# Kernel tuning notes

Hardware: AMD Instinct MI355X
Metric: run time of the kernel (lower is better)

## Reference

```python
import jax, jax.numpy as jnp
import numpy as np

B = 1024           # number of drug pairs (graphs per side)
ATOMS = 64         # atoms per molecule
N = B * ATOMS      # total atoms per side
H = 512            # hidden_size * number_of_molecules
FFN_H = 2048
OUT = 86           # num_tasks


def setup_inputs() -> dict:
    key = jax.random.key(0)
    ks = jax.random.split(key, 12)
    inv = 1.0 / np.sqrt(H)
    inv2 = 1.0 / np.sqrt(2 * H)
    invf = 1.0 / np.sqrt(FFN_H)
    return {
        "left_output": jax.random.normal(ks[0], (B, H), jnp.float32),
        "right_output": jax.random.normal(ks[1], (B, H), jnp.float32),
        "left_atom": jax.random.normal(ks[2], (N, H), jnp.float32),
        "right_atom": jax.random.normal(ks[3], (N, H), jnp.float32),
        "left_batch": jnp.arange(N, dtype=jnp.int32) // ATOMS,
        "right_batch": jnp.arange(N, dtype=jnp.int32) // ATOMS,
        "noise": jax.random.uniform(ks[4], (B, H), jnp.float32),
        "w_i_w": jax.random.normal(ks[5], (H, H), jnp.float32) * inv,
        "w_i_b": jnp.zeros((H,), jnp.float32),
        "prj_i_w": jax.random.normal(ks[6], (H, H), jnp.float32) * inv,
        "prj_i_b": jnp.zeros((H,), jnp.float32),
        "ffn1_w": jax.random.normal(ks[7], (2 * H, FFN_H), jnp.float32) * inv2,
        "ffn1_b": jnp.zeros((FFN_H,), jnp.float32),
        "ffn2_w": jax.random.normal(ks[8], (FFN_H, OUT), jnp.float32) * invf,
        "ffn2_b": jnp.zeros((OUT,), jnp.float32),
    }


def _seg_softmax(s, seg, num_segments):
    m = jax.ops.segment_max(s, seg, num_segments=num_segments)
    e = jnp.exp(s - m[seg])
    z = jax.ops.segment_sum(e, seg, num_segments=num_segments)
    return e / z[seg]


def reference(left_output, right_output, left_atom, right_atom,
              left_batch, right_batch, noise,
              w_i_w, w_i_b, prj_i_w, prj_i_b,
              ffn1_w, ffn1_b, ffn2_w, ffn2_b):
    # repeat_interleave(left_output, degree(right_batch)) == gather by segment id
    left_align = left_output[right_batch]    # [N_r, H]
    right_align = right_output[left_batch]   # [N_l, H]

    # cross-molecule coattention scores (elementwise product + reduce)
    left_scores = jnp.sum((left_atom @ w_i_w + w_i_b) * (right_align @ prj_i_w + prj_i_b), axis=-1)
    left_scores = _seg_softmax(left_scores, left_batch, B)
    right_scores = jnp.sum((right_atom @ w_i_w + w_i_b) * (left_align @ prj_i_w + prj_i_b), axis=-1)
    right_scores = _seg_softmax(right_scores, right_batch, B)

    # attention-weighted global add pool
    h_output = jax.ops.segment_sum(left_atom * right_align * left_scores[:, None], left_batch, num_segments=B)
    t_output = jax.ops.segment_sum(right_atom * left_align * right_scores[:, None], right_batch, num_segments=B)

    # sign-directed noise perturbation (same noise for both sides, as in original)
    nrm = jnp.maximum(jnp.linalg.norm(noise, axis=-1, keepdims=True), 1e-12)
    noise_n = noise / nrm
    h_pert = h_output + jnp.sign(h_output) * noise_n * 0.1
    t_pert = t_output + jnp.sign(t_output) * noise_n * 0.1

    pair = jnp.concatenate([h_pert, t_pert], axis=-1)  # [B, 2H]
    hid = jax.nn.relu(pair @ ffn1_w + ffn1_b)
    output = hid @ ffn2_w + ffn2_b  # training mode: raw logits, no sigmoid
    return (output, h_output, h_pert, left_scores, right_scores, left_output, right_output)
```

## Files before the change

kernel.cpp:

```cpp
#include <hip/hip_runtime.h>
#include <hip/hip_bf16.h>

#define B_ 1024
#define H_ 512
#define N_ (B_ * 64)
#define FFN_ 2048
#define OUT_ 86

typedef __bf16 bf16_t;
typedef __attribute__((ext_vector_type(8))) __bf16 bf16x8;
typedef __attribute__((ext_vector_type(4))) float f32x4;

__device__ __forceinline__ float wred_sum(float v) {
#pragma unroll
  for (int m = 32; m; m >>= 1) v += __shfl_xor(v, m);
  return v;
}
__device__ __forceinline__ float wred_max(float v) {
#pragma unroll
  for (int m = 32; m; m >>= 1) v = fmaxf(v, __shfl_xor(v, m));
  return v;
}

__device__ __forceinline__ void gload_lds16(const void* g, void* l) {
  __builtin_amdgcn_global_load_lds((const __attribute__((address_space(1))) unsigned int*)g,
                                   (__attribute__((address_space(3))) unsigned int*)l, 16, 0, 0);
}

__global__ void k_prep(const float* __restrict__ w_i_w, const float* __restrict__ w_i_b,
                       const float* __restrict__ prj_w, const float* __restrict__ prj_b,
                       float* __restrict__ dv, float* __restrict__ ev, float* __restrict__ c0) {
  int b = blockIdx.x, l = threadIdx.x;
  float s = 0.f;
  if (b < 512) {
    for (int h = l; h < H_; h += 64) s += w_i_w[b * H_ + h] * prj_b[h];
    s = wred_sum(s);
    if (l == 0) dv[b] = s;
  } else if (b < 1024) {
    int j = b - 512;
    for (int h = l; h < H_; h += 64) s += prj_w[j * H_ + h] * w_i_b[h];
    s = wred_sum(s);
    if (l == 0) ev[j] = s;
  } else {
    for (int h = l; h < H_; h += 64) s += w_i_b[h] * prj_b[h];
    s = wred_sum(s);
    if (l == 0) c0[0] = s;
  }
}

__global__ void k_cvec(const float* __restrict__ ro, const float* __restrict__ lo,
                       const float* __restrict__ ev, const float* __restrict__ c0,
                       float* __restrict__ cL, float* __restrict__ cR) {
  int b = blockIdx.x, side = blockIdx.y, l = threadIdx.x;
  const float* x = side ? lo : ro;
  float s = 0.f;
  for (int j = l; j < H_; j += 64) s += x[b * H_ + j] * ev[j];
  s = wred_sum(s);
  if (l == 0) (side ? cR : cL)[b] = s + c0[0];
}

template <bool BT, bool BIAS, bool RELU>
__global__ __launch_bounds__(256) void gemm64(const float* __restrict__ A, const float* __restrict__ Bm,
                                              const float* __restrict__ bias, float* __restrict__ C,
                                              int M, int N, int K) {
  __shared__ float As[16][68];
  __shared__ float Bs[16][68];
  const int bm = blockIdx.x * 64, bn = blockIdx.y * 64;
  const int t = threadIdx.x;
  const int tx = t & 15, ty = t >> 4;
  float acc[4][4] = {};
  for (int k0 = 0; k0 < K; k0 += 16) {
#pragma unroll
    for (int i = 0; i < 4; i++) {
      int m = (t >> 4) + i * 16;
      As[t & 15][m] = A[(size_t)(bm + m) * K + k0 + (t & 15)];
    }
    if (BT) {
#pragma unroll
      for (int i = 0; i < 4; i++) {
        int n = (t >> 4) + i * 16;
        Bs[t & 15][n] = Bm[(size_t)(bn + n) * K + k0 + (t & 15)];
      }
    } else {
#pragma unroll
      for (int i = 0; i < 4; i++) {
        int kk = (t >> 6) + i * 4;
        Bs[kk][t & 63] = Bm[(size_t)(k0 + kk) * N + bn + (t & 63)];
      }
    }
    __syncthreads();
#pragma unroll
    for (int kk = 0; kk < 16; kk++) {
      float4 av = *(const float4*)&As[kk][ty * 4];
      float4 bv = *(const float4*)&Bs[kk][tx * 4];
      float a_[4] = {av.x, av.y, av.z, av.w};
      float b_[4] = {bv.x, bv.y, bv.z, bv.w};
#pragma unroll
      for (int i = 0; i < 4; i++)
#pragma unroll
        for (int j = 0; j < 4; j++) acc[i][j] += a_[i] * b_[j];
    }
    __syncthreads();
  }
#pragma unroll
  for (int i = 0; i < 4; i++) {
    int m = bm + ty * 4 + i;
    float tmp[4];
#pragma unroll
    for (int j = 0; j < 4; j++) {
      float x = acc[i][j];
      if (BIAS) x += bias[bn + tx * 4 + j];
      if (RELU) x = fmaxf(x, 0.f);
      tmp[j] = x;
    }
    float4 v;
    v.x = tmp[0]; v.y = tmp[1]; v.z = tmp[2]; v.w = tmp[3];
    *(float4*)&C[(size_t)m * N + bn + tx * 4] = v;
  }
}

__global__ __launch_bounds__(512, 2) void k_atoms(const float* __restrict__ atomL, const float* __restrict__ atomR,
                                                  const float* __restrict__ uL, const float* __restrict__ uR,
                                                  const float* __restrict__ cL, const float* __restrict__ cR,
                                                  float* __restrict__ scoresL, float* __restrict__ scoresR,
                                                  float* __restrict__ pL, float* __restrict__ pR) {
  const int b = blockIdx.x, side = blockIdx.y;
  const float* __restrict__ atom = side ? atomR : atomL;
  const float* __restrict__ u = side ? uR : uL;
  const float cb = (side ? cR : cL)[b];
  float* __restrict__ scores = side ? scoresR : scoresL;
  float* __restrict__ p = side ? pR : pL;

  const int t = threadIdx.x, wave = t >> 6, lane = t & 63;
  const int colA = lane * 4, colB = 256 + lane * 4;

  __shared__ float s_lds[64];
  __shared__ float pp_lds[8][512];

  float a[8][8];
  float ur[8];
  const float* base = atom + ((size_t)b * 64 + wave * 8) * H_;
#pragma unroll
  for (int ai = 0; ai < 8; ai++) {
    *(float4*)&a[ai][0] = *(const float4*)&base[(size_t)ai * H_ + colA];
    *(float4*)&a[ai][4] = *(const float4*)&base[(size_t)ai * H_ + colB];
  }
  *(float4*)&ur[0] = *(const float4*)&u[(size_t)b * H_ + colA];
  *(float4*)&ur[4] = *(const float4*)&u[(size_t)b * H_ + colB];

#pragma unroll
  for (int ai = 0; ai < 8; ai++) {
    float dot = 0.f;
#pragma unroll
    for (int j = 0; j < 8; j++) dot += a[ai][j] * ur[j];
    dot = wred_sum(dot);
    if (lane == 0) s_lds[wave * 8 + ai] = dot + cb;
  }
  __syncthreads();
  if (wave == 0) {
    float s = s_lds[lane];
    float mx = wred_max(s);
    float e = expf(s - mx);
    float z = wred_sum(e);
    float w = e / z;
    s_lds[lane] = w;
    scores[(size_t)b * 64 + lane] = w;
  }
  __syncthreads();
  float pp[8] = {};
#pragma unroll
  for (int ai = 0; ai < 8; ai++) {
    float w = s_lds[wave * 8 + ai];
#pragma unroll
    for (int j = 0; j < 8; j++) pp[j] += w * a[ai][j];
  }
#pragma unroll
  for (int j = 0; j < 4; j++) {
    pp_lds[wave][colA + j] = pp[j];
    pp_lds[wave][colB + j] = pp[4 + j];
  }
  __syncthreads();
  float s = 0.f;
#pragma unroll
  for (int w2 = 0; w2 < 8; w2++) s += pp_lds[w2][t];
  p[(size_t)b * H_ + t] = s;
}

__global__ __launch_bounds__(512) void k_pert(const float* __restrict__ lo, const float* __restrict__ ro,
                                              const float* __restrict__ noise,
                                              const float* __restrict__ pL, const float* __restrict__ pR,
                                              float* __restrict__ h_out, float* __restrict__ h_pert,
                                              bf16_t* __restrict__ pairbf) {
  const int b = blockIdx.x, t = threadIdx.x;
  float nv = noise[(size_t)b * H_ + t];
  float sq = nv * nv;
  sq = wred_sum(sq);
  __shared__ float red[8];
  if ((t & 63) == 0) red[t >> 6] = sq;
  __syncthreads();
  float tot = 0.f;
#pragma unroll
  for (int i = 0; i < 8; i++) tot += red[i];
  float nrm = fmaxf(sqrtf(tot), 1e-12f);
  float nn = nv / nrm * 0.1f;
  float h = ro[(size_t)b * H_ + t] * pL[(size_t)b * H_ + t];
  float tt = lo[(size_t)b * H_ + t] * pR[(size_t)b * H_ + t];
  float sh = (h > 0.f) ? 1.f : ((h < 0.f) ? -1.f : 0.f);
  float st = (tt > 0.f) ? 1.f : ((tt < 0.f) ? -1.f : 0.f);
  float hp = h + sh * nn;
  float tp = tt + st * nn;
  h_out[(size_t)b * H_ + t] = h;
  h_pert[(size_t)b * H_ + t] = hp;
  pairbf[(size_t)b * 1024 + t] = (bf16_t)hp;
  pairbf[(size_t)b * 1024 + 512 + t] = (bf16_t)tp;
}

__global__ __launch_bounds__(256) void k_w1t(const float* __restrict__ W1, bf16_t* __restrict__ W1t) {
  __shared__ float tile[32][33];
  const int bx = blockIdx.x;
  const int by = blockIdx.y;
  const int tx = threadIdx.x & 31, ty = threadIdx.x >> 5;
#pragma unroll
  for (int i = ty; i < 32; i += 8)
    tile[i][tx] = W1[(size_t)(by * 32 + i) * FFN_ + bx * 32 + tx];
  __syncthreads();
#pragma unroll
  for (int i = ty; i < 32; i += 8)
    W1t[(size_t)(bx * 32 + i) * 1024 + by * 32 + tx] = (bf16_t)tile[tx][i];
}

__global__ __launch_bounds__(256) void k_ffn1(const bf16_t* __restrict__ Abf, const bf16_t* __restrict__ Bt,
                                              const float* __restrict__ bias, float* __restrict__ C) {
  __shared__ bf16_t As[64 * 64];
  __shared__ bf16_t Bs[64 * 64];
  const int bm = blockIdx.x * 64, bn = blockIdx.y * 64;
  const int t = threadIdx.x;
  const int lane = t & 63, wave = t >> 6;
  const int wm = wave & 1, wn = wave >> 1;
  const int l15 = lane & 15, l4 = lane >> 4;
  f32x4 acc[2][2] = {{{0.f, 0.f, 0.f, 0.f}, {0.f, 0.f, 0.f, 0.f}},
                     {{0.f, 0.f, 0.f, 0.f}, {0.f, 0.f, 0.f, 0.f}}};

  for (int k0 = 0; k0 < 1024; k0 += 64) {
#pragma unroll
    for (int r = 0; r < 2; r++) {
      const int off = (r * 256 + t) * 16;
      const int row = off >> 7;
      const int g = (off >> 4) & 7;
      const int scb = ((g ^ (row & 7)) << 4);
      gload_lds16((const char*)Abf + (size_t)(bm + row) * 2048 + k0 * 2 + scb, (char*)As + off);
      gload_lds16((const char*)Bt + (size_t)(bn + row) * 2048 + k0 * 2 + scb, (char*)Bs + off);
    }
    __syncthreads();
#pragma unroll
    for (int ks = 0; ks < 2; ks++) {
      const int ar0 = wm * 32 + l15, ar1 = ar0 + 16;
      const int br0 = wn * 32 + l15, br1 = br0 + 16;
      const int gA = ks * 4 + l4;
      bf16x8 a0 = *(const bf16x8*)((const char*)As + ar0 * 128 + ((gA ^ (ar0 & 7)) << 4));
      bf16x8 a1 = *(const bf16x8*)((const char*)As + ar1 * 128 + ((gA ^ (ar1 & 7)) << 4));
      bf16x8 b0 = *(const bf16x8*)((const char*)Bs + br0 * 128 + ((gA ^ (br0 & 7)) << 4));
      bf16x8 b1 = *(const bf16x8*)((const char*)Bs + br1 * 128 + ((gA ^ (br1 & 7)) << 4));
      acc[0][0] = __builtin_amdgcn_mfma_f32_16x16x32_bf16(a0, b0, acc[0][0], 0, 0, 0);
      acc[0][1] = __builtin_amdgcn_mfma_f32_16x16x32_bf16(a0, b1, acc[0][1], 0, 0, 0);
      acc[1][0] = __builtin_amdgcn_mfma_f32_16x16x32_bf16(a1, b0, acc[1][0], 0, 0, 0);
      acc[1][1] = __builtin_amdgcn_mfma_f32_16x16x32_bf16(a1, b1, acc[1][1], 0, 0, 0);
    }
    __syncthreads();
  }
#pragma unroll
  for (int mi = 0; mi < 2; mi++)
#pragma unroll
    for (int nj = 0; nj < 2; nj++)
#pragma unroll
      for (int r = 0; r < 4; r++) {
        const int m = bm + wm * 32 + mi * 16 + l4 * 4 + r;
        const int n = bn + wn * 32 + nj * 16 + l15;
        float v = acc[mi][nj][r] + bias[n];
        C[(size_t)m * FFN_ + n] = fmaxf(v, 0.f);
      }
}

__global__ void k_w2t(const float* __restrict__ W2, float* __restrict__ W2t) {
  int idx = blockIdx.x * 256 + threadIdx.x;
  if (idx < OUT_ * FFN_) {
    int n = idx / FFN_, k = idx % FFN_;
    W2t[idx] = W2[(size_t)k * OUT_ + n];
  }
}

__global__ __launch_bounds__(256) void k_ffn2(const float* __restrict__ hid, const float* __restrict__ W2t,
                                              const float* __restrict__ b2, float* __restrict__ out) {
  const int b0 = blockIdx.x * 2;
  const int t = threadIdx.x, wave = t >> 6, lane = t & 63;
  float4 h0[8], h1[8];
  const float* r0 = hid + (size_t)b0 * FFN_;
#pragma unroll
  for (int j = 0; j < 8; j++) {
    h0[j] = *(const float4*)&r0[lane * 4 + j * 256];
    h1[j] = *(const float4*)&r0[FFN_ + lane * 4 + j * 256];
  }
  for (int n = wave; n < OUT_; n += 4) {
    const float* wrow = W2t + (size_t)n * FFN_;
    float s0 = 0.f, s1 = 0.f;
#pragma unroll
    for (int j = 0; j < 8; j++) {
      float4 w4 = *(const float4*)&wrow[lane * 4 + j * 256];
      s0 += w4.x * h0[j].x + w4.y * h0[j].y + w4.z * h0[j].z + w4.w * h0[j].w;
      s1 += w4.x * h1[j].x + w4.y * h1[j].y + w4.z * h1[j].z + w4.w * h1[j].w;
    }
    s0 = wred_sum(s0);
    s1 = wred_sum(s1);
    if (lane == 0) {
      out[(size_t)b0 * OUT_ + n] = s0 + b2[n];
      out[(size_t)(b0 + 1) * OUT_ + n] = s1 + b2[n];
    }
  }
}

extern "C" void kernel_launch(void* const* d_in, const int* in_sizes, int n_in,
                              void* d_out, int out_size, void* d_ws, size_t ws_size,
                              hipStream_t stream) {
  const float* lo = (const float*)d_in[0];
  const float* ro = (const float*)d_in[1];
  const float* la = (const float*)d_in[2];
  const float* ra = (const float*)d_in[3];
  const float* noise = (const float*)d_in[6];
  const float* w_i_w = (const float*)d_in[7];
  const float* w_i_b = (const float*)d_in[8];
  const float* prj_w = (const float*)d_in[9];
  const float* prj_b = (const float*)d_in[10];
  const float* W1 = (const float*)d_in[11];
  const float* b1 = (const float*)d_in[12];
  const float* W2 = (const float*)d_in[13];
  const float* b2 = (const float*)d_in[14];

  float* out = (float*)d_out;
  float* o_logits = out;
  float* o_hout  = out + 88064;
  float* o_hpert = o_hout + 524288;
  float* o_ls    = o_hpert + 524288;
  float* o_rs    = o_ls + 65536;
  float* o_lo    = o_rs + 65536;
  float* o_ro    = o_lo + 524288;

  float* ws = (float*)d_ws;
  float* Mt   = ws; ws += 512 * 512;
  float* uL   = ws; ws += B_ * H_;
  float* uR   = ws; ws += B_ * H_;
  float* pL   = ws; ws += B_ * H_;
  float* pR   = ws; ws += B_ * H_;
  float* hid  = ws; ws += B_ * FFN_;
  float* W2t  = ws; ws += OUT_ * FFN_;
  bf16_t* pairbf = (bf16_t*)ws; ws += B_ * 1024 / 2;
  bf16_t* W1t    = (bf16_t*)ws; ws += FFN_ * 1024 / 2;
  float* dv   = ws; ws += 512;
  float* ev   = ws; ws += 512;
  float* cL   = ws; ws += 1024;
  float* cR   = ws; ws += 1024;
  float* c0   = ws; ws += 4;

  k_prep<<<1025, 64, 0, stream>>>(w_i_w, w_i_b, prj_w, prj_b, dv, ev, c0);
  gemm64<true, false, false><<<dim3(8, 8), 256, 0, stream>>>(w_i_w, prj_w, nullptr, Mt, 512, 512, 512);
  gemm64<true, true, false><<<dim3(16, 8), 256, 0, stream>>>(ro, Mt, dv, uL, 1024, 512, 512);
  gemm64<true, true, false><<<dim3(16, 8), 256, 0, stream>>>(lo, Mt, dv, uR, 1024, 512, 512);
  k_cvec<<<dim3(1024, 2), 64, 0, stream>>>(ro, lo, ev, c0, cL, cR);
  k_w1t<<<dim3(64, 32), 256, 0, stream>>>(W1, W1t);
  k_atoms<<<dim3(1024, 2), 512, 0, stream>>>(la, ra, uL, uR, cL, cR, o_ls, o_rs, pL, pR);
  k_pert<<<1024, 512, 0, stream>>>(lo, ro, noise, pL, pR, o_hout, o_hpert, pairbf);
  k_ffn1<<<dim3(16, 32), 256, 0, stream>>>(pairbf, W1t, b1, hid);
  k_w2t<<<688, 256, 0, stream>>>(W2, W2t);
  k_ffn2<<<512, 256, 0, stream>>>(hid, W2t, b2, o_logits);
  hipMemcpyAsync(o_lo, lo, (size_t)B_ * H_ * 4, hipMemcpyDeviceToDevice, stream);
  hipMemcpyAsync(o_ro, ro, (size_t)B_ * H_ * 4, hipMemcpyDeviceToDevice, stream);
}
```

Baseline: 189.7 us.

## Stream atom tiles through double-buffered LDS with online softmax in k_atoms

k_atoms no longer holds all 64 atom rows in registers. It loads 8-row chunks into double-buffered LDS with global_load_lds and computes the segment softmax online, using a running max and rescaled sums. Lower register pressure allows raising launch bounds to 4 blocks per CU, and prefetching overlaps loads with compute. The cost is three barriers per chunk and 32KB of LDS per block, which may limit occupancy and add synchronisation overhead.

```diff
diff --git a/kernel.cpp b/kernel.cpp
--- a/kernel.cpp
+++ b/kernel.cpp
@@ -1,5 +1,6 @@
 #include <hip/hip_runtime.h>
 #include <hip/hip_bf16.h>
+#include <float.h>
 
 #define B_ 1024
 #define H_ 512
@@ -26,6 +27,8 @@
   __builtin_amdgcn_global_load_lds((const __attribute__((address_space(1))) unsigned int*)g,
                                    (__attribute__((address_space(3))) unsigned int*)l, 16, 0, 0);
 }
+
+#define BARRAW() do { asm volatile("s_waitcnt lgkmcnt(0)" ::: "memory"); __builtin_amdgcn_s_barrier(); } while (0)
 
 __global__ void k_prep(const float* __restrict__ w_i_w, const float* __restrict__ w_i_b,
                        const float* __restrict__ prj_w, const float* __restrict__ prj_b,
@@ -119,7 +122,7 @@
   }
 }
 
-__global__ __launch_bounds__(512, 2) void k_atoms(const float* __restrict__ atomL, const float* __restrict__ atomR,
+__global__ __launch_bounds__(512, 4) void k_atoms(const float* __restrict__ atomL, const float* __restrict__ atomR,
                                                   const float* __restrict__ uL, const float* __restrict__ uR,
                                                   const float* __restrict__ cL, const float* __restrict__ cR,
                                                   float* __restrict__ scoresL, float* __restrict__ scoresR,
@@ -132,58 +135,76 @@
   float* __restrict__ p = side ? pR : pL;
 
   const int t = threadIdx.x, wave = t >> 6, lane = t & 63;
-  const int colA = lane * 4, colB = 256 + lane * 4;
-
-  __shared__ float s_lds[64];
-  __shared__ float pp_lds[8][512];
-
-  float a[8][8];
-  float ur[8];
-  const float* base = atom + ((size_t)b * 64 + wave * 8) * H_;
-#pragma unroll
-  for (int ai = 0; ai < 8; ai++) {
-    *(float4*)&a[ai][0] = *(const float4*)&base[(size_t)ai * H_ + colA];
-    *(float4*)&a[ai][4] = *(const float4*)&base[(size_t)ai * H_ + colB];
-  }
-  *(float4*)&ur[0] = *(const float4*)&u[(size_t)b * H_ + colA];
-  *(float4*)&ur[4] = *(const float4*)&u[(size_t)b * H_ + colB];
-
-#pragma unroll
-  for (int ai = 0; ai < 8; ai++) {
-    float dot = 0.f;
-#pragma unroll
-    for (int j = 0; j < 8; j++) dot += a[ai][j] * ur[j];
-    dot = wred_sum(dot);
-    if (lane == 0) s_lds[wave * 8 + ai] = dot + cb;
-  }
-  __syncthreads();
-  if (wave == 0) {
-    float s = s_lds[lane];
-    float mx = wred_max(s);
-    float e = expf(s - mx);
-    float z = wred_sum(e);
-    float w = e / z;
-    s_lds[lane] = w;
-    scores[(size_t)b * 64 + lane] = w;
-  }
-  __syncthreads();
-  float pp[8] = {};
-#pragma unroll
-  for (int ai = 0; ai < 8; ai++) {
-    float w = s_lds[wave * 8 + ai];
-#pragma unroll
-    for (int j = 0; j < 8; j++) pp[j] += w * a[ai][j];
-  }
-#pragma unroll
-  for (int j = 0; j < 4; j++) {
-    pp_lds[wave][colA + j] = pp[j];
-    pp_lds[wave][colB + j] = pp[4 + j];
-  }
-  __syncthreads();
-  float s = 0.f;
-#pragma unroll
-  for (int w2 = 0; w2 < 8; w2++) s += pp_lds[w2][t];
-  p[(size_t)b * H_ + t] = s;
+
+  __shared__ float buf[2][8 * 512];
+  __shared__ float s_all[64];
+  __shared__ float e_lds[8];
+  __shared__ float r_lds, z_lds;
+
+  const char* gbase = (const char*)(atom + (size_t)b * 64 * H_);
+
+  {
+    char* lb = (char*)&buf[0][0];
+    gload_lds16(gbase + t * 16, lb + t * 16);
+    gload_lds16(gbase + (512 + t) * 16, lb + (512 + t) * 16);
+  }
+  f32x4 u0 = *(const f32x4*)&u[(size_t)b * H_ + lane * 4];
+  f32x4 u1 = *(const f32x4*)&u[(size_t)b * H_ + 256 + lane * 4];
+
+  float pacc = 0.f;
+  float m_old = -FLT_MAX;
+  float Z = 0.f;
+
+  asm volatile("s_waitcnt vmcnt(0)" ::: "memory");
+  BARRAW();
+
+  int cur = 0;
+#pragma unroll
+  for (int c = 0; c < 8; c++) {
+    if (c < 7) {
+      const char* gb = gbase + (size_t)(c + 1) * 8 * 2048;
+      char* lb = (char*)&buf[cur ^ 1][0];
+      gload_lds16(gb + t * 16, lb + t * 16);
+      gload_lds16(gb + (512 + t) * 16, lb + (512 + t) * 16);
+    }
+    const float* bc = &buf[cur][0];
+    {
+      f32x4 a0 = *(const f32x4*)(bc + wave * 512 + lane * 4);
+      f32x4 a1 = *(const f32x4*)(bc + wave * 512 + 256 + lane * 4);
+      float dot = a0.x * u0.x + a0.y * u0.y + a0.z * u0.z + a0.w * u0.w +
+                  a1.x * u1.x + a1.y * u1.y + a1.z * u1.z + a1.w * u1.w;
+      dot = wred_sum(dot);
+      if (lane == 0) s_all[c * 8 + wave] = dot + cb;
+    }
+    BARRAW();
+    if (wave == 0) {
+      float val = (lane < 8) ? s_all[c * 8 + lane] : -FLT_MAX;
+      float cmax = wred_max(val);
+      float m_new = fmaxf(m_old, cmax);
+      float r = expf(m_old - m_new);
+      float e = (lane < 8) ? expf(val - m_new) : 0.f;
+      float csum = wred_sum(e);
+      Z = Z * r + csum;
+      m_old = m_new;
+      if (lane < 8) e_lds[lane] = e;
+      if (lane == 0) { r_lds = r; z_lds = Z; }
+    }
+    BARRAW();
+    {
+      float r = r_lds;
+      float pp = pacc * r;
+#pragma unroll
+      for (int i = 0; i < 8; i++) pp += e_lds[i] * bc[i * 512 + t];
+      pacc = pp;
+    }
+    asm volatile("s_waitcnt vmcnt(0)" ::: "memory");
+    BARRAW();
+    cur ^= 1;
+  }
+
+  float zf = z_lds;
+  p[(size_t)b * H_ + t] = pacc / zf;
+  if (wave == 0) scores[(size_t)b * 64 + lane] = expf(s_all[lane] - m_old) / zf;
 }
 
 __global__ __launch_bounds__(512) void k_pert(const float* __restrict__ lo, const float* __restrict__ ro,
```

Measured after the change: 240.6 us. 1.27x slower.

## Use one wave per molecule with online softmax and reassociate score projection GEMMs

Applied to the files above, without the earlier changes.

The atom kernel now assigns one wavefront per (side, molecule) and streams the 64 atoms in chunks of 8. It keeps a running max and sum (online softmax) and accumulates the weighted pool in registers, which removes the block-wide LDS reductions and __syncthreads. The projection chain is reassociated as (x·prj_w + prj_b)·w_i_wᵀ, with both sides batched into one GEMM launch per step. This drops the separate W·Pᵀ GEMM and the dv bias vector. The trade-offs are more serialized per-wave work, fewer blocks in flight, and a 2048-row intermediate T buffer.

```diff
diff --git a/kernel.cpp b/kernel.cpp
--- a/kernel.cpp
+++ b/kernel.cpp
@@ -1,5 +1,6 @@
 #include <hip/hip_runtime.h>
 #include <hip/hip_bf16.h>
+#include <float.h>
 
 #define B_ 1024
 #define H_ 512
@@ -16,31 +17,21 @@
   for (int m = 32; m; m >>= 1) v += __shfl_xor(v, m);
   return v;
 }
-__device__ __forceinline__ float wred_max(float v) {
-#pragma unroll
-  for (int m = 32; m; m >>= 1) v = fmaxf(v, __shfl_xor(v, m));
-  return v;
-}
 
 __device__ __forceinline__ void gload_lds16(const void* g, void* l) {
   __builtin_amdgcn_global_load_lds((const __attribute__((address_space(1))) unsigned int*)g,
                                    (__attribute__((address_space(3))) unsigned int*)l, 16, 0, 0);
 }
 
-__global__ void k_prep(const float* __restrict__ w_i_w, const float* __restrict__ w_i_b,
+__global__ void k_prep(const float* __restrict__ w_i_b,
                        const float* __restrict__ prj_w, const float* __restrict__ prj_b,
-                       float* __restrict__ dv, float* __restrict__ ev, float* __restrict__ c0) {
+                       float* __restrict__ ev, float* __restrict__ c0) {
   int b = blockIdx.x, l = threadIdx.x;
   float s = 0.f;
   if (b < 512) {
-    for (int h = l; h < H_; h += 64) s += w_i_w[b * H_ + h] * prj_b[h];
+    for (int h = l; h < H_; h += 64) s += prj_w[b * H_ + h] * w_i_b[h];
     s = wred_sum(s);
-    if (l == 0) dv[b] = s;
-  } else if (b < 1024) {
-    int j = b - 512;
-    for (int h = l; h < H_; h += 64) s += prj_w[j * H_ + h] * w_i_b[h];
-    s = wred_sum(s);
-    if (l == 0) ev[j] = s;
+    if (l == 0) ev[b] = s;
   } else {
     for (int h = l; h < H_; h += 64) s += w_i_b[h] * prj_b[h];
     s = wred_sum(s);
@@ -59,13 +50,15 @@
   if (l == 0) (side ? cR : cL)[b] = s + c0[0];
 }
 
-template <bool BT, bool BIAS, bool RELU>
-__global__ __launch_bounds__(256) void gemm64(const float* __restrict__ A, const float* __restrict__ Bm,
+template <bool BT, bool BIAS>
+__global__ __launch_bounds__(256) void gemm64(const float* __restrict__ A1, const float* __restrict__ A2,
+                                              int M1, const float* __restrict__ Bm,
                                               const float* __restrict__ bias, float* __restrict__ C,
-                                              int M, int N, int K) {
+                                              int N, int K) {
   __shared__ float As[16][68];
   __shared__ float Bs[16][68];
   const int bm = blockIdx.x * 64, bn = blockIdx.y * 64;
+  const float* __restrict__ A = (bm < M1) ? (A1 + (size_t)bm * K) : (A2 + (size_t)(bm - M1) * K);
   const int t = threadIdx.x;
   const int tx = t & 15, ty = t >> 4;
   float acc[4][4] = {};
@@ -73,7 +66,7 @@
 #pragma unroll
     for (int i = 0; i < 4; i++) {
       int m = (t >> 4) + i * 16;
-      As[t & 15][m] = A[(size_t)(bm + m) * K + k0 + (t & 15)];
+      As[t & 15][m] = A[(size_t)m * K + k0 + (t & 15)];
     }
     if (BT) {
 #pragma unroll
@@ -110,7 +103,6 @@
     for (int j = 0; j < 4; j++) {
       float x = acc[i][j];
       if (BIAS) x += bias[bn + tx * 4 + j];
-      if (RELU) x = fmaxf(x, 0.f);
       tmp[j] = x;
     }
     float4 v;
@@ -119,71 +111,80 @@
   }
 }
 
-__global__ __launch_bounds__(512, 2) void k_atoms(const float* __restrict__ atomL, const float* __restrict__ atomR,
-                                                  const float* __restrict__ uL, const float* __restrict__ uR,
-                                                  const float* __restrict__ cL, const float* __restrict__ cR,
-                                                  float* __restrict__ scoresL, float* __restrict__ scoresR,
-                                                  float* __restrict__ pL, float* __restrict__ pR) {
-  const int b = blockIdx.x, side = blockIdx.y;
+__global__ __launch_bounds__(256, 2) void k_atoms2(const float* __restrict__ atomL, const float* __restrict__ atomR,
+                                                   const float* __restrict__ uLR,
+                                                   const float* __restrict__ cL, const float* __restrict__ cR,
+                                                   float* __restrict__ scoresL, float* __restrict__ scoresR,
+                                                   float* __restrict__ pL, float* __restrict__ pR) {
+  const int gw = blockIdx.x * 4 + (threadIdx.x >> 6);
+  const int side = gw >> 10;
+  const int b = gw & 1023;
+  const int lane = threadIdx.x & 63;
+
   const float* __restrict__ atom = side ? atomR : atomL;
-  const float* __restrict__ u = side ? uR : uL;
   const float cb = (side ? cR : cL)[b];
   float* __restrict__ scores = side ? scoresR : scoresL;
   float* __restrict__ p = side ? pR : pL;
 
-  const int t = threadIdx.x, wave = t >> 6, lane = t & 63;
-  const int colA = lane * 4, colB = 256 + lane * 4;
-
-  __shared__ float s_lds[64];
-  __shared__ float pp_lds[8][512];
-
-  float a[8][8];
+  const float* __restrict__ u = uLR + (size_t)gw * H_;
   float ur[8];
-  const float* base = atom + ((size_t)b * 64 + wave * 8) * H_;
-#pragma unroll
-  for (int ai = 0; ai < 8; ai++) {
-    *(float4*)&a[ai][0] = *(const float4*)&base[(size_t)ai * H_ + colA];
-    *(float4*)&a[ai][4] = *(const float4*)&base[(size_t)ai * H_ + colB];
-  }
-  *(float4*)&ur[0] = *(const float4*)&u[(size_t)b * H_ + colA];
-  *(float4*)&ur[4] = *(const float4*)&u[(size_t)b * H_ + colB];
-
-#pragma unroll
-  for (int ai = 0; ai < 8; ai++) {
-    float dot = 0.f;
-#pragma unroll
-    for (int j = 0; j < 8; j++) dot += a[ai][j] * ur[j];
-    dot = wred_sum(dot);
-    if (lane == 0) s_lds[wave * 8 + ai] = dot + cb;
-  }
-  __syncthreads();
-  if (wave == 0) {
-    float s = s_lds[lane];
-    float mx = wred_max(s);
-    float e = expf(s - mx);
-    float z = wred_sum(e);
-    float w = e / z;
-    s_lds[lane] = w;
-    scores[(size_t)b * 64 + lane] = w;
-  }
-  __syncthreads();
-  float pp[8] = {};
-#pragma unroll
-  for (int ai = 0; ai < 8; ai++) {
-    float w = s_lds[wave * 8 + ai];
-#pragma unroll
-    for (int j = 0; j < 8; j++) pp[j] += w * a[ai][j];
-  }
-#pragma unroll
-  for (int j = 0; j < 4; j++) {
-    pp_lds[wave][colA + j] = pp[j];
-    pp_lds[wave][colB + j] = pp[4 + j];
-  }
-  __syncthreads();
-  float s = 0.f;
-#pragma unroll
-  for (int w2 = 0; w2 < 8; w2++) s += pp_lds[w2][t];
-  p[(size_t)b * H_ + t] = s;
+  *(f32x4*)&ur[0] = *(const f32x4*)&u[lane * 8];
+  *(f32x4*)&ur[4] = *(const f32x4*)&u[lane * 8 + 4];
+
+  const float* __restrict__ base = atom + (size_t)b * 64 * H_ + lane * 8;
+
+  float q[8] = {};
+  float m_run = -FLT_MAX, z_run = 0.f;
+  float myraw = 0.f;
+
+#pragma unroll
+  for (int c = 0; c < 8; c++) {
+    float a[8][8];
+#pragma unroll
+    for (int i = 0; i < 8; i++) {
+      const float* rp = base + (size_t)(c * 8 + i) * H_;
+      *(f32x4*)&a[i][0] = *(const f32x4*)rp;
+      *(f32x4*)&a[i][4] = *(const f32x4*)(rp + 4);
+    }
+    float d[8];
+#pragma unroll
+    for (int i = 0; i < 8; i++) {
+      float s = 0.f;
+#pragma unroll
+      for (int j = 0; j < 8; j++) s += a[i][j] * ur[j];
+      d[i] = s;
+    }
+#pragma unroll
+    for (int i = 0; i < 8; i++) d[i] = wred_sum(d[i]) + cb;
+#pragma unroll
+    for (int i = 0; i < 8; i++) myraw = (lane == c * 8 + i) ? d[i] : myraw;
+    float mc = d[0];
+#pragma unroll
+    for (int i = 1; i < 8; i++) mc = fmaxf(mc, d[i]);
+    float m_new = fmaxf(m_run, mc);
+    float r = __expf(m_run - m_new);
+    float e[8];
+    float zc = 0.f;
+#pragma unroll
+    for (int i = 0; i < 8; i++) { e[i] = __expf(d[i] - m_new); zc += e[i]; }
+    z_run = z_run * r + zc;
+    m_run = m_new;
+#pragma unroll
+    for (int j = 0; j < 8; j++) q[j] *= r;
+#pragma unroll
+    for (int i = 0; i < 8; i++)
+#pragma unroll
+      for (int j = 0; j < 8; j++) q[j] += e[i] * a[i][j];
+  }
+
+  const float zinv = 1.f / z_run;
+  float outp[8];
+#pragma unroll
+  for (int j = 0; j < 8; j++) outp[j] = q[j] * zinv;
+  float* pd = p + (size_t)b * H_ + lane * 8;
+  *(f32x4*)&pd[0] = *(const f32x4*)&outp[0];
+  *(f32x4*)&pd[4] = *(const f32x4*)&outp[4];
+  scores[(size_t)b * 64 + lane] = __expf(myraw - m_run) * zinv;
 }
 
 __global__ __launch_bounds__(512) void k_pert(const float* __restrict__ lo, const float* __restrict__ ro,
@@ -345,28 +346,25 @@
   float* o_ro    = o_lo + 524288;
 
   float* ws = (float*)d_ws;
-  float* Mt   = ws; ws += 512 * 512;
-  float* uL   = ws; ws += B_ * H_;
-  float* uR   = ws; ws += B_ * H_;
+  float* T    = ws; ws += 2048 * 512;
+  float* uLR  = ws; ws += 2048 * 512;
   float* pL   = ws; ws += B_ * H_;
   float* pR   = ws; ws += B_ * H_;
   float* hid  = ws; ws += B_ * FFN_;
   float* W2t  = ws; ws += OUT_ * FFN_;
   bf16_t* pairbf = (bf16_t*)ws; ws += B_ * 1024 / 2;
   bf16_t* W1t    = (bf16_t*)ws; ws += FFN_ * 1024 / 2;
-  float* dv   = ws; ws += 512;
   float* ev   = ws; ws += 512;
   float* cL   = ws; ws += 1024;
   float* cR   = ws; ws += 1024;
   float* c0   = ws; ws += 4;
 
-  k_prep<<<1025, 64, 0, stream>>>(w_i_w, w_i_b, prj_w, prj_b, dv, ev, c0);
-  gemm64<true, false, false><<<dim3(8, 8), 256, 0, stream>>>(w_i_w, prj_w, nullptr, Mt, 512, 512, 512);
-  gemm64<true, true, false><<<dim3(16, 8), 256, 0, stream>>>(ro, Mt, dv, uL, 1024, 512, 512);
-  gemm64<true, true, false><<<dim3(16, 8), 256, 0, stream>>>(lo, Mt, dv, uR, 1024, 512, 512);
+  k_prep<<<513, 64, 0, stream>>>(w_i_b, prj_w, prj_b, ev, c0);
+  gemm64<false, true><<<dim3(32, 8), 256, 0, stream>>>(ro, lo, 1024, prj_w, prj_b, T, 512, 512);
+  gemm64<true, false><<<dim3(32, 8), 256, 0, stream>>>(T, T, 1 << 30, w_i_w, nullptr, uLR, 512, 512);
   k_cvec<<<dim3(1024, 2), 64, 0, stream>>>(ro, lo, ev, c0, cL, cR);
   k_w1t<<<dim3(64, 32), 256, 0, stream>>>(W1, W1t);
-  k_atoms<<<dim3(1024, 2), 512, 0, stream>>>(la, ra, uL, uR, cL, cR, o_ls, o_rs, pL, pR);
+  k_atoms2<<<512, 256, 0, stream>>>(la, ra, uLR, cL, cR, o_ls, o_rs, pL, pR);
   k_pert<<<1024, 512, 0, stream>>>(lo, ro, noise, pL, pR, o_hout, o_hpert, pairbf);
   k_ffn1<<<dim3(16, 32), 256, 0, stream>>>(pairbf, W1t, b1, hid);
   k_w2t<<<688, 256, 0, stream>>>(W2, W2t);
```

New measurement: 173.3 us. 8.7% less time.
